# Performance work log

Measured on AMD Instinct MI355X. Metric: run time of the kernel, lower is better.

The kernel has to match this reference:

```python
import jax, jax.numpy as jnp
import numpy as np

B, L, E = 4, 2048, 1024
H, HS = 16, 64  # head_num, head_size; E == H*HS


def setup_inputs() -> dict:
    key = jax.random.key(0)
    k1, k2, k3 = jax.random.split(key, 3)
    x = jax.random.normal(k1, (B, L, E), dtype=jnp.float32)
    W_attn = jax.random.normal(k2, (E, 3 * H * HS), dtype=jnp.float32) * (E ** -0.5)
    W_ffn = jax.random.normal(k3, (H * HS, E), dtype=jnp.float32) * ((H * HS) ** -0.5)
    return {"x": x, "W_attn": W_attn, "W_ffn": W_ffn}


def reference(x, W_attn, W_ffn):
    b, l, _ = x.shape
    z = x @ W_attn  # [B, L, 3*H*HS]
    # NOTE: original splits as (k, q, v) in that order
    k, q, v = jnp.split(z, 3, axis=2)
    k = k.reshape(b, l, H, HS).transpose(0, 2, 1, 3)  # [B,H,L,HS]
    q = q.reshape(b, l, H, HS).transpose(0, 2, 1, 3)
    v = v.reshape(b, l, H, HS).transpose(0, 2, 1, 3)
    # scores[i, j] = k_i . q_j (k plays the row role, q the column role)
    scores = jnp.einsum('bhid,bhjd->bhij', k, q) / (HS ** 0.5)
    idx = jnp.arange(l)
    causal = idx[None, :] > idx[:, None]  # True where j > i (masked out)
    scores = jnp.where(causal[None, None], -jnp.inf, scores)
    attn = jax.nn.softmax(scores, axis=-1)  # softmax over j (the q index)
    y = jnp.einsum('bhij,bhjd->bhid', attn, v)  # [B,H,L,HS]
    y = y.transpose(0, 2, 1, 3).reshape(b, l, H * HS)
    return y @ W_ffn
```

## Files before the change

kernel.cpp:

```cpp
#include <hip/hip_runtime.h>
#include <hip/hip_bf16.h>

typedef __attribute__((ext_vector_type(8))) short bf16x8;
typedef __attribute__((ext_vector_type(4))) float f32x4;

__device__ __forceinline__ short f2b(float f) {
    unsigned u = __builtin_bit_cast(unsigned, f);
    unsigned r = (u + 0x7FFFu + ((u >> 16) & 1u)) >> 16;
    return (short)r;
}

__device__ __forceinline__ unsigned cvt_pk_bf16(float lo, float hi) {
    unsigned r;
    asm("v_cvt_pk_bf16_f32 %0, %1, %2" : "=v"(r) : "v"(lo), "v"(hi));
    return r;
}

__device__ __forceinline__ float fexp2(float x) {
    float r;
    asm("v_exp_f32 %0, %1" : "=v"(r) : "v"(x));
    return r;
}

__device__ __forceinline__ void gload_lds16(const void* g, void* l) {
    __builtin_amdgcn_global_load_lds((const __attribute__((address_space(1))) unsigned*)g,
                                     (__attribute__((address_space(3))) unsigned*)l, 16, 0, 0);
}

__global__ void conv_swz(const float* __restrict__ in, short* __restrict__ out, long nch) {
    long i = (long)blockIdx.x * blockDim.x + threadIdx.x;
    long stride = (long)gridDim.x * blockDim.x;
    for (; i < nch; i += stride) {
        long m = i >> 7;
        int ch = (int)(i & 127);
        int p = (ch & ~7) | ((ch ^ (int)m) & 7);
        const float4* s = (const float4*)(in + i * 8);
        float4 a = s[0], b = s[1];
        bf16x8 ov;
        ov[0] = f2b(a.x); ov[1] = f2b(a.y); ov[2] = f2b(a.z); ov[3] = f2b(a.w);
        ov[4] = f2b(b.x); ov[5] = f2b(b.y); ov[6] = f2b(b.z); ov[7] = f2b(b.w);
        *(bf16x8*)(out + (m << 10) + p * 8) = ov;
    }
}

__global__ void transpose_swz(const float* __restrict__ in, short* __restrict__ outT, int R, int C) {
    __shared__ float t[32][33];
    int c0 = blockIdx.x * 32, r0 = blockIdx.y * 32;
    int tx = threadIdx.x, ty = threadIdx.y;
    #pragma unroll
    for (int j = 0; j < 4; ++j)
        t[ty + j * 8][tx] = in[(long)(r0 + ty + j * 8) * C + c0 + tx];
    __syncthreads();
    #pragma unroll
    for (int j = 0; j < 4; ++j) {
        int n = c0 + ty + j * 8;
        int k = r0 + tx;
        int kp = (k & ~63) | ((((k >> 3) ^ n) & 7) << 3) | (k & 7);
        outT[(long)n * R + kp] = f2b(t[tx][ty + j * 8]);
    }
}

template<int MODE>
__launch_bounds__(256, 4)
__global__ void gemm_nt(const short* __restrict__ A, const short* __restrict__ Bt,
                        int M, int N, int K,
                        short* __restrict__ qrole, short* __restrict__ krole,
                        short* __restrict__ vT, float* __restrict__ out) {
    __shared__ __align__(16) short As[128][64];
    __shared__ __align__(16) short Bs[128][64];
    const int tid = threadIdx.x;
    const int lane = tid & 63;
    const int wid = tid >> 6;
    const int wm = wid >> 1, wn = wid & 1;
    const int m0 = blockIdx.y * 128, n0 = blockIdx.x * 128;
    const int r16 = lane & 15, g = lane >> 4;
    const int sw = r16 & 7;
    const char* Ab = (const char*)A;
    const char* Bb = (const char*)Bt;
    const long Kb = (long)K * 2;
    f32x4 acc[4][4] = {};
    for (int k0 = 0; k0 < K; k0 += 64) {
        #pragma unroll
        for (int it = 0; it < 4; ++it) {
            int id = it * 256 + tid;
            int r = id >> 3, cch = id & 7;
            gload_lds16(Ab + (long)(m0 + r) * Kb + k0 * 2 + cch * 16, (char*)As + id * 16);
            gload_lds16(Bb + (long)(n0 + r) * Kb + k0 * 2 + cch * 16, (char*)Bs + id * 16);
        }
        __syncthreads();
        #pragma unroll
        for (int kk = 0; kk < 2; ++kk) {
            bf16x8 af[4], bfr[4];
            #pragma unroll
            for (int m = 0; m < 4; ++m)
                af[m] = *(const bf16x8*)&As[wm * 64 + m * 16 + r16][((kk * 4 + g) ^ sw) * 8];
            #pragma unroll
            for (int n = 0; n < 4; ++n)
                bfr[n] = *(const bf16x8*)&Bs[wn * 64 + n * 16 + r16][((kk * 4 + g) ^ sw) * 8];
            #pragma unroll
            for (int m = 0; m < 4; ++m)
                #pragma unroll
                for (int n = 0; n < 4; ++n)
                    acc[m][n] = __builtin_amdgcn_mfma_f32_16x16x32_bf16(af[m], bfr[n], acc[m][n], 0, 0, 0);
        }
        __syncthreads();
    }
    #pragma unroll
    for (int m = 0; m < 4; ++m) {
        #pragma unroll
        for (int n = 0; n < 4; ++n) {
            #pragma unroll
            for (int r = 0; r < 4; ++r) {
                int row = m0 + wm * 64 + m * 16 + g * 4 + r;
                int col = n0 + wn * 64 + n * 16 + r16;
                float v = acc[m][n][r];
                if (MODE == 0) {
                    int which = col >> 10, cc = col & 1023;
                    int h = cc >> 6, d = cc & 63;
                    int b = row >> 11, li = row & 2047;
                    int bh = b * 16 + h;
                    if (which == 0)      qrole[((long)bh * 2048 + li) * 64 + d] = f2b(v * 0.18033688f);
                    else if (which == 1) krole[((long)bh * 2048 + li) * 64 + (d ^ ((li & 7) << 3))] = f2b(v);
                    else                 vT[((long)bh * 64 + d) * 2048 + ((li & ~63) | ((li & 63) ^ ((d & 7) << 3)))] = f2b(v);
                } else {
                    out[(long)row * N + col] = v;
                }
            }
        }
    }
}

__launch_bounds__(256, 4)
__global__ void attn_kernel(const short* __restrict__ qrole, const short* __restrict__ krole,
                            const short* __restrict__ vT, short* __restrict__ y) {
    __shared__ __align__(16) short K_lds[2][64][64];
    __shared__ __align__(16) short V_lds[2][64][64];
    __shared__ __align__(16) short P_lds[4][16][64];
    const int tid = threadIdx.x, lane = tid & 63, w = tid >> 6;
    const int r16 = lane & 15, g = lane >> 4;
    const int idb = blockIdx.x;
    const int bh = idb & 63;
    const int u = idb >> 8;
    const int a = (idb >> 6) & 3;
    const int c = (u == 0) ? (15 - a) : (u == 1) ? a : (u == 2) ? (11 - a) : (4 + a);
    const int q0 = c << 7;
    const int T = 2 * c + 2;
    const short* qb = qrole + (long)bh * (2048 * 64);
    const char* kbyte = (const char*)(krole + (long)bh * (2048 * 64));
    const char* vbyte = (const char*)(vT + (long)bh * (64 * 2048));
    const int b = bh >> 4, h = bh & 15;

    bf16x8 qf[2][2];
    #pragma unroll
    for (int m = 0; m < 2; ++m)
        #pragma unroll
        for (int ks = 0; ks < 2; ++ks)
            qf[m][ks] = *(const bf16x8*)&qb[(long)(q0 + m * 64 + w * 16 + r16) * 64 + ks * 32 + g * 8];

    f32x4 o[2][4] = {};
    float mr[2], lr[2];
    #pragma unroll
    for (int m = 0; m < 2; ++m) { mr[m] = -1e30f; lr[m] = 0.f; }

    const int rr = tid >> 3, cch = tid & 7;
    const char* kg0 = kbyte + rr * 128 + cch * 16;
    const char* kg1 = kbyte + (32 + rr) * 128 + cch * 16;
    const char* vg0 = vbyte + rr * 4096 + cch * 16;
    const char* vg1 = vbyte + (32 + rr) * 4096 + cch * 16;
    char* Kb_ = (char*)&K_lds[0][0][0];
    char* Vb_ = (char*)&V_lds[0][0][0];
    const int ld0 = tid * 16, ld1 = (256 + tid) * 16;

    gload_lds16(kg0, Kb_ + ld0);
    gload_lds16(kg1, Kb_ + ld1);
    gload_lds16(vg0, Vb_ + ld0);
    gload_lds16(vg1, Vb_ + ld1);

    const int psw = (r16 & 7) << 4;
    char* prow = (char*)&P_lds[w][r16][0];

    for (int t = 0; t < T; ++t) {
        __syncthreads();
        const int cur = t & 1;
        if (t + 1 < T) {
            long adv = (long)(t + 1) * 8192;
            long advv = (long)(t + 1) * 128;
            char* kdst = Kb_ + (cur ^ 1) * 8192;
            char* vdst = Vb_ + (cur ^ 1) * 8192;
            gload_lds16(kg0 + adv, kdst + ld0);
            gload_lds16(kg1 + adv, kdst + ld1);
            gload_lds16(vg0 + advv, vdst + ld0);
            gload_lds16(vg1 + advv, vdst + ld1);
        }
        const int jt = t << 6;
        const char* kbase = Kb_ + cur * 8192;
        const char* vbase = Vb_ + cur * 8192;

        #pragma unroll
        for (int m = 0; m < 2; ++m) {
            const int qbase = q0 + m * 64 + w * 16;
            if (jt > qbase + 15) continue;

            f32x4 s[4] = {};
            __builtin_amdgcn_s_setprio(1);
            #pragma unroll
            for (int ks = 0; ks < 2; ++ks)
                #pragma unroll
                for (int n = 0; n < 4; ++n) {
                    bf16x8 kf = *(const bf16x8*)(kbase + (n * 16 + r16) * 128 + ((ks * 64 + g * 16) ^ psw));
                    s[n] = __builtin_amdgcn_mfma_f32_16x16x32_bf16(kf, qf[m][ks], s[n], 0, 0, 0);
                }
            __builtin_amdgcn_s_setprio(0);
            if (jt + 63 > qbase) {
                const int i = qbase + r16;
                #pragma unroll
                for (int n = 0; n < 4; ++n)
                    #pragma unroll
                    for (int r = 0; r < 4; ++r)
                        if (jt + n * 16 + g * 4 + r > i) s[n][r] = -1e30f;
            }
            float t0 = fmaxf(fmaxf(s[0][0], s[0][1]), fmaxf(s[0][2], s[0][3]));
            float t1 = fmaxf(fmaxf(s[1][0], s[1][1]), fmaxf(s[1][2], s[1][3]));
            float t2 = fmaxf(fmaxf(s[2][0], s[2][1]), fmaxf(s[2][2], s[2][3]));
            float t3 = fmaxf(fmaxf(s[3][0], s[3][1]), fmaxf(s[3][2], s[3][3]));
            float tm = fmaxf(fmaxf(t0, t1), fmaxf(t2, t3));
            tm = fmaxf(tm, __shfl_xor(tm, 16));
            tm = fmaxf(tm, __shfl_xor(tm, 32));
            if (__any(tm > mr[m] + 11.5f)) {
                float mn = fmaxf(mr[m], tm);
                float sc = fexp2(mr[m] - mn);
                mr[m] = mn;
                lr[m] *= sc;
                float scr[4];
                #pragma unroll
                for (int r = 0; r < 4; ++r) scr[r] = __shfl(sc, (g << 2) + r);
                #pragma unroll
                for (int nd = 0; nd < 4; ++nd)
                    #pragma unroll
                    for (int r = 0; r < 4; ++r)
                        o[m][nd][r] *= scr[r];
            }
            float p[4][4];
            #pragma unroll
            for (int n = 0; n < 4; ++n) {
                p[n][0] = fexp2(s[n][0] - mr[m]);
                p[n][1] = fexp2(s[n][1] - mr[m]);
                p[n][2] = fexp2(s[n][2] - mr[m]);
                p[n][3] = fexp2(s[n][3] - mr[m]);
                unsigned w0 = cvt_pk_bf16(p[n][0], p[n][1]);
                unsigned w1 = cvt_pk_bf16(p[n][2], p[n][3]);
                unsigned long long dw = ((unsigned long long)w1 << 32) | w0;
                *(unsigned long long*)(prow + ((n * 32 + g * 8) ^ psw)) = dw;
            }
            float l0 = (p[0][0] + p[0][1]) + (p[0][2] + p[0][3]);
            float l1 = (p[1][0] + p[1][1]) + (p[1][2] + p[1][3]);
            float l2 = (p[2][0] + p[2][1]) + (p[2][2] + p[2][3]);
            float l3 = (p[3][0] + p[3][1]) + (p[3][2] + p[3][3]);
            float lsum = (l0 + l1) + (l2 + l3);
            lsum += __shfl_xor(lsum, 16);
            lsum += __shfl_xor(lsum, 32);
            lr[m] += lsum;
            __builtin_amdgcn_s_setprio(1);
            #pragma unroll
            for (int ks = 0; ks < 2; ++ks) {
                bf16x8 pf = *(const bf16x8*)(prow + ((ks * 64 + g * 16) ^ psw));
                #pragma unroll
                for (int nd = 0; nd < 4; ++nd) {
                    bf16x8 vf = *(const bf16x8*)(vbase + (nd * 16 + r16) * 128 + ((ks * 64 + g * 16) ^ psw));
                    o[m][nd] = __builtin_amdgcn_mfma_f32_16x16x32_bf16(pf, vf, o[m][nd], 0, 0, 0);
                }
            }
            __builtin_amdgcn_s_setprio(0);
        }
    }
    #pragma unroll
    for (int m = 0; m < 2; ++m) {
        float inv[4];
        #pragma unroll
        for (int r = 0; r < 4; ++r) inv[r] = 1.0f / __shfl(lr[m], (g << 2) + r);
        const int li0 = q0 + m * 64 + w * 16 + (g << 2);
        #pragma unroll
        for (int nd = 0; nd < 4; ++nd)
            #pragma unroll
            for (int r = 0; r < 4; ++r) {
                int li = li0 + r;
                int sub = ((nd * 2 + (r16 >> 3)) ^ li) & 7;
                int kp = h * 64 + sub * 8 + (r16 & 7);
                y[(long)(b * 2048 + li) * 1024 + kp] = f2b(o[m][nd][r] * inv[r]);
            }
    }
}

extern "C" void kernel_launch(void* const* d_in, const int* in_sizes, int n_in,
                              void* d_out, int out_size, void* d_ws, size_t ws_size,
                              hipStream_t stream) {
    const float* x  = (const float*)d_in[0];
    const float* Wa = (const float*)d_in[1];
    const float* Wf = (const float*)d_in[2];
    float* out = (float*)d_out;
    char* ws = (char*)d_ws;
    short* xb  = (short*)(ws);
    short* wab = (short*)(ws + (16l << 20));
    short* wfb = (short*)(ws + (22l << 20));
    short* qr  = (short*)(ws + (24l << 20));
    short* kr  = (short*)(ws + (40l << 20));
    short* vt  = (short*)(ws + (56l << 20));

    conv_swz<<<2048, 256, 0, stream>>>(x, xb, (long)8192 * 128);
    transpose_swz<<<dim3(96, 32), dim3(32, 8), 0, stream>>>(Wa, wab, 1024, 3072);
    transpose_swz<<<dim3(32, 32), dim3(32, 8), 0, stream>>>(Wf, wfb, 1024, 1024);
    gemm_nt<0><<<dim3(24, 64), 256, 0, stream>>>(xb, wab, 8192, 3072, 1024, qr, kr, vt, nullptr);
    attn_kernel<<<1024, 256, 0, stream>>>(qr, kr, vt, xb);
    gemm_nt<1><<<dim3(8, 64), 256, 0, stream>>>(xb, wfb, 8192, 1024, 1024, nullptr, nullptr, nullptr, out);
}
```

Measured before the change: 174.5 us.

## Split long causal query chunks across two blocks and merge partial softmax results

Query chunks 8-15 are each split into two KV-range segments handled by separate blocks, which write unnormalized bf16 partial outputs plus row max and sum to workspace. A new merge kernel rescales and combines each pair into y. This evens out per-block work under the causal mask and raises the block count to 1536, aiming to shorten the tail. The cost is an extra launch, extra global traffic, and bf16 rounding of the partial outputs. The split path only runs when the workspace is large enough.

```diff
diff --git a/kernel.cpp b/kernel.cpp
--- a/kernel.cpp
+++ b/kernel.cpp
@@ -8,6 +8,10 @@
     unsigned u = __builtin_bit_cast(unsigned, f);
     unsigned r = (u + 0x7FFFu + ((u >> 16) & 1u)) >> 16;
     return (short)r;
+}
+
+__device__ __forceinline__ float b2f(short s) {
+    return __builtin_bit_cast(float, ((unsigned)(unsigned short)s) << 16);
 }
 
 __device__ __forceinline__ unsigned cvt_pk_bf16(float lo, float hi) {
@@ -130,9 +134,14 @@
     }
 }
 
+__device__ const int g_uc[24]   = {15,15, 7,14,14, 6,13,13, 5,12,12, 4,11,11, 3,10,10, 2, 9, 9, 1, 8, 8, 0};
+__device__ const int g_ukind[24]= { 1, 2, 0, 1, 2, 0, 1, 2, 0, 1, 2, 0, 1, 2, 0, 1, 2, 0, 1, 2, 0, 1, 2, 0};
+
+template<int SPLIT>
 __launch_bounds__(256, 4)
 __global__ void attn_kernel(const short* __restrict__ qrole, const short* __restrict__ krole,
-                            const short* __restrict__ vT, short* __restrict__ y) {
+                            const short* __restrict__ vT, short* __restrict__ y,
+                            short* __restrict__ pO, float2* __restrict__ pML) {
     __shared__ __align__(16) short K_lds[2][64][64];
     __shared__ __align__(16) short V_lds[2][64][64];
     __shared__ __align__(16) short P_lds[4][16][64];
@@ -140,11 +149,19 @@
     const int r16 = lane & 15, g = lane >> 4;
     const int idb = blockIdx.x;
     const int bh = idb & 63;
-    const int u = idb >> 8;
-    const int a = (idb >> 6) & 3;
-    const int c = (u == 0) ? (15 - a) : (u == 1) ? a : (u == 2) ? (11 - a) : (4 + a);
+    int c, kind, t0, Tn;
+    if (SPLIT) {
+        const int u = idb >> 6;
+        c = g_uc[u];
+        kind = g_ukind[u];
+        t0 = (kind == 2) ? (c + 1) : 0;
+        Tn = (kind == 0) ? (2 * c + 2) : (c + 1);
+    } else {
+        const int u = idb >> 8, a = (idb >> 6) & 3;
+        c = (u == 0) ? (15 - a) : (u == 1) ? a : (u == 2) ? (11 - a) : (4 + a);
+        kind = 0; t0 = 0; Tn = 2 * c + 2;
+    }
     const int q0 = c << 7;
-    const int T = 2 * c + 2;
     const short* qb = qrole + (long)bh * (2048 * 64);
     const char* kbyte = (const char*)(krole + (long)bh * (2048 * 64));
     const char* vbyte = (const char*)(vT + (long)bh * (64 * 2048));
@@ -171,18 +188,19 @@
     char* Vb_ = (char*)&V_lds[0][0][0];
     const int ld0 = tid * 16, ld1 = (256 + tid) * 16;
 
-    gload_lds16(kg0, Kb_ + ld0);
-    gload_lds16(kg1, Kb_ + ld1);
-    gload_lds16(vg0, Vb_ + ld0);
-    gload_lds16(vg1, Vb_ + ld1);
+    gload_lds16(kg0 + (long)t0 * 8192, Kb_ + ld0);
+    gload_lds16(kg1 + (long)t0 * 8192, Kb_ + ld1);
+    gload_lds16(vg0 + (long)t0 * 128, Vb_ + ld0);
+    gload_lds16(vg1 + (long)t0 * 128, Vb_ + ld1);
 
     const int psw = (r16 & 7) << 4;
     char* prow = (char*)&P_lds[w][r16][0];
-
-    for (int t = 0; t < T; ++t) {
+    const int tend = t0 + Tn;
+
+    for (int t = t0; t < tend; ++t) {
         __syncthreads();
-        const int cur = t & 1;
-        if (t + 1 < T) {
+        const int cur = (t - t0) & 1;
+        if (t + 1 < tend) {
             long adv = (long)(t + 1) * 8192;
             long advv = (long)(t + 1) * 128;
             char* kdst = Kb_ + (cur ^ 1) * 8192;
@@ -211,7 +229,7 @@
                     s[n] = __builtin_amdgcn_mfma_f32_16x16x32_bf16(kf, qf[m][ks], s[n], 0, 0, 0);
                 }
             __builtin_amdgcn_s_setprio(0);
-            if (jt + 63 > qbase) {
+            if (kind != 1 && jt + 63 > qbase) {
                 const int i = qbase + r16;
                 #pragma unroll
                 for (int n = 0; n < 4; ++n)
@@ -219,11 +237,11 @@
                     for (int r = 0; r < 4; ++r)
                         if (jt + n * 16 + g * 4 + r > i) s[n][r] = -1e30f;
             }
-            float t0 = fmaxf(fmaxf(s[0][0], s[0][1]), fmaxf(s[0][2], s[0][3]));
-            float t1 = fmaxf(fmaxf(s[1][0], s[1][1]), fmaxf(s[1][2], s[1][3]));
-            float t2 = fmaxf(fmaxf(s[2][0], s[2][1]), fmaxf(s[2][2], s[2][3]));
-            float t3 = fmaxf(fmaxf(s[3][0], s[3][1]), fmaxf(s[3][2], s[3][3]));
-            float tm = fmaxf(fmaxf(t0, t1), fmaxf(t2, t3));
+            float t0_ = fmaxf(fmaxf(s[0][0], s[0][1]), fmaxf(s[0][2], s[0][3]));
+            float t1_ = fmaxf(fmaxf(s[1][0], s[1][1]), fmaxf(s[1][2], s[1][3]));
+            float t2_ = fmaxf(fmaxf(s[2][0], s[2][1]), fmaxf(s[2][2], s[2][3]));
+            float t3_ = fmaxf(fmaxf(s[3][0], s[3][1]), fmaxf(s[3][2], s[3][3]));
+            float tm = fmaxf(fmaxf(t0_, t1_), fmaxf(t2_, t3_));
             tm = fmaxf(tm, __shfl_xor(tm, 16));
             tm = fmaxf(tm, __shfl_xor(tm, 32));
             if (__any(tm > mr[m] + 11.5f)) {
@@ -273,21 +291,75 @@
             __builtin_amdgcn_s_setprio(0);
         }
     }
-    #pragma unroll
-    for (int m = 0; m < 2; ++m) {
-        float inv[4];
-        #pragma unroll
-        for (int r = 0; r < 4; ++r) inv[r] = 1.0f / __shfl(lr[m], (g << 2) + r);
-        const int li0 = q0 + m * 64 + w * 16 + (g << 2);
-        #pragma unroll
-        for (int nd = 0; nd < 4; ++nd)
+
+    if (kind == 0) {
+        #pragma unroll
+        for (int m = 0; m < 2; ++m) {
+            float inv[4];
+            #pragma unroll
+            for (int r = 0; r < 4; ++r) inv[r] = 1.0f / __shfl(lr[m], (g << 2) + r);
+            const int li0 = q0 + m * 64 + w * 16 + (g << 2);
+            #pragma unroll
+            for (int nd = 0; nd < 4; ++nd)
+                #pragma unroll
+                for (int r = 0; r < 4; ++r) {
+                    int li = li0 + r;
+                    int sub = ((nd * 2 + (r16 >> 3)) ^ li) & 7;
+                    int kp = h * 64 + sub * 8 + (r16 & 7);
+                    y[(long)(b * 2048 + li) * 1024 + kp] = f2b(o[m][nd][r] * inv[r]);
+                }
+        }
+    } else {
+        const int seg = kind - 1, sc_ = c - 8;
+        const long slot = ((long)bh * 8 + sc_) * 2 + seg;
+        #pragma unroll
+        for (int m = 0; m < 2; ++m) {
+            float mv[4], lv[4];
             #pragma unroll
             for (int r = 0; r < 4; ++r) {
-                int li = li0 + r;
-                int sub = ((nd * 2 + (r16 >> 3)) ^ li) & 7;
-                int kp = h * 64 + sub * 8 + (r16 & 7);
-                y[(long)(b * 2048 + li) * 1024 + kp] = f2b(o[m][nd][r] * inv[r]);
-            }
+                mv[r] = __shfl(mr[m], (g << 2) + r);
+                lv[r] = __shfl(lr[m], (g << 2) + r);
+            }
+            const int row0 = m * 64 + w * 16 + (g << 2);
+            #pragma unroll
+            for (int nd = 0; nd < 4; ++nd)
+                #pragma unroll
+                for (int r = 0; r < 4; ++r)
+                    pO[(slot * 128 + row0 + r) * 64 + nd * 16 + r16] = f2b(o[m][nd][r]);
+            if (r16 == 0) {
+                #pragma unroll
+                for (int r = 0; r < 4; ++r)
+                    pML[slot * 128 + row0 + r] = make_float2(mv[r], lv[r]);
+            }
+        }
+    }
+}
+
+__global__ void merge_kernel(const short* __restrict__ pO, const float2* __restrict__ pML,
+                             short* __restrict__ y) {
+    const int bh = blockIdx.x >> 3, sc_ = blockIdx.x & 7;
+    const int row = threadIdx.x >> 1, hf = threadIdx.x & 1;
+    const long slotA = ((long)bh * 8 + sc_) * 2, slotB = slotA + 1;
+    const float2 mlA = pML[slotA * 128 + row];
+    const float2 mlB = pML[slotB * 128 + row];
+    const float ms = fmaxf(mlA.x, mlB.x);
+    const float eA = fexp2(mlA.x - ms), eB = fexp2(mlB.x - ms);
+    const float inv = 1.0f / (mlA.y * eA + mlB.y * eB);
+    const float fA = eA * inv, fB = eB * inv;
+    const int c = 8 + sc_;
+    const int li = (c << 7) + row;
+    const int b = bh >> 4, h = bh & 15;
+    #pragma unroll
+    for (int ch = 0; ch < 4; ++ch) {
+        const int d0 = hf * 32 + ch * 8;
+        bf16x8 a = *(const bf16x8*)&pO[(slotA * 128 + row) * 64 + d0];
+        bf16x8 bb = *(const bf16x8*)&pO[(slotB * 128 + row) * 64 + d0];
+        bf16x8 res;
+        #pragma unroll
+        for (int j = 0; j < 8; ++j)
+            res[j] = f2b(b2f(a[j]) * fA + b2f(bb[j]) * fB);
+        const int kp0 = h * 64 + ((((d0 >> 3) ^ li) & 7) << 3);
+        *(bf16x8*)&y[(long)(b * 2048 + li) * 1024 + kp0] = res;
     }
 }
 
@@ -305,11 +377,18 @@
     short* qr  = (short*)(ws + (24l << 20));
     short* kr  = (short*)(ws + (40l << 20));
     short* vt  = (short*)(ws + (56l << 20));
+    short* pO  = (short*)(ws + (72l << 20));
+    float2* pML = (float2*)(ws + (89l << 20));
 
     conv_swz<<<2048, 256, 0, stream>>>(x, xb, (long)8192 * 128);
     transpose_swz<<<dim3(96, 32), dim3(32, 8), 0, stream>>>(Wa, wab, 1024, 3072);
     transpose_swz<<<dim3(32, 32), dim3(32, 8), 0, stream>>>(Wf, wfb, 1024, 1024);
     gemm_nt<0><<<dim3(24, 64), 256, 0, stream>>>(xb, wab, 8192, 3072, 1024, qr, kr, vt, nullptr);
-    attn_kernel<<<1024, 256, 0, stream>>>(qr, kr, vt, xb);
+    if (ws_size >= (91ull << 20)) {
+        attn_kernel<1><<<1536, 256, 0, stream>>>(qr, kr, vt, xb, pO, pML);
+        merge_kernel<<<512, 256, 0, stream>>>(pO, pML, xb);
+    } else {
+        attn_kernel<0><<<1024, 256, 0, stream>>>(qr, kr, vt, xb, nullptr, nullptr);
+    }
     gemm_nt<1><<<dim3(8, 64), 256, 0, stream>>>(xb, wfb, 8192, 1024, 1024, nullptr, nullptr, nullptr, out);
 }
```

Result: slower. 182.0 us (+4.3%).

## Use 256x256-tile double-buffered GEMM kernel for QKV projection

Applied to the files above, without the earlier changes.

Replaces the 128x128 QKV projection GEMM with a dedicated 512-thread kernel using 256x256 output tiles, 128KB of double-buffered LDS filled by direct global-to-LDS loads, and an interleaved stage/read/MFMA schedule with priority hints. Blocks are remapped across M/N for better cache locality. The larger tile cuts global and LDS traffic per FLOP and overlaps loads with compute, at the cost of one block per CU and only 384 blocks for 256 CUs, which leaves a wave-quantization tail. The output GEMM is de-templated, and some attention variables are renamed.

```diff
diff --git a/kernel.cpp b/kernel.cpp
--- a/kernel.cpp
+++ b/kernel.cpp
@@ -60,12 +60,130 @@
     }
 }
 
-template<int MODE>
+__launch_bounds__(512, 1)
+__global__ void gemm256_nt(const short* __restrict__ A, const short* __restrict__ Bt,
+                           short* __restrict__ qrole, short* __restrict__ krole,
+                           short* __restrict__ vT) {
+    __shared__ __align__(16) char ldsb[131072];
+    const int tid = threadIdx.x, lane = tid & 63, wid = tid >> 6;
+    const int wm = wid >> 2, wn = wid & 3;
+    const int r16 = lane & 15, g = lane >> 4;
+    const int sw8 = r16 & 7;
+    const int swz = (blockIdx.x & 7) * 48 + (blockIdx.x >> 3);
+    const int m0 = (swz & 31) * 256, n0 = (swz >> 5) * 256;
+    const long Kb2 = 2048;
+    const char* Ab = (const char*)A;
+    const char* Bb = (const char*)Bt;
+    const int c0 = tid, c1 = tid + 512;
+    const int sr0 = c0 >> 3, so0 = (c0 & 7) * 16;
+    const int sr1 = c1 >> 3, so1 = (c1 & 7) * 16;
+
+    f32x4 acc[8][4] = {};
+    bf16x8 af[4][2], bfr[4][2];
+
+#define STAGE_A(tt, h) do { \
+        const char* sb_ = Ab + (long)(m0 + (h) * 128) * Kb2 + (long)(tt) * 128; \
+        char* db_ = ldsb + ((tt) & 1) * 65536 + (h) * 16384; \
+        gload_lds16(sb_ + (long)sr0 * Kb2 + so0, db_ + c0 * 16); \
+        gload_lds16(sb_ + (long)sr1 * Kb2 + so1, db_ + c1 * 16); } while (0)
+#define STAGE_B(tt, h) do { \
+        const char* sb_ = Bb + (long)(n0 + (h) * 128) * Kb2 + (long)(tt) * 128; \
+        char* db_ = ldsb + ((tt) & 1) * 65536 + 32768 + (h) * 16384; \
+        gload_lds16(sb_ + (long)sr0 * Kb2 + so0, db_ + c0 * 16); \
+        gload_lds16(sb_ + (long)sr1 * Kb2 + so1, db_ + c1 * 16); } while (0)
+#define READ_A(buf, mh) do { \
+        const char* base_ = ldsb + (buf) * 65536; \
+        _Pragma("unroll") \
+        for (int f_ = 0; f_ < 4; ++f_) { \
+            const char* rp_ = base_ + (wm * 128 + (mh) * 64 + f_ * 16 + r16) * 128; \
+            af[f_][0] = *(const bf16x8*)(rp_ + ((g ^ sw8) * 16)); \
+            af[f_][1] = *(const bf16x8*)(rp_ + (((4 + g) ^ sw8) * 16)); } } while (0)
+#define READ_B(buf) do { \
+        const char* base_ = ldsb + (buf) * 65536 + 32768; \
+        _Pragma("unroll") \
+        for (int f_ = 0; f_ < 4; ++f_) { \
+            const char* rp_ = base_ + (wn * 64 + f_ * 16 + r16) * 128; \
+            bfr[f_][0] = *(const bf16x8*)(rp_ + ((g ^ sw8) * 16)); \
+            bfr[f_][1] = *(const bf16x8*)(rp_ + (((4 + g) ^ sw8) * 16)); } } while (0)
+#define DO_MFMA(mh, nh) do { \
+        __builtin_amdgcn_s_setprio(1); \
+        _Pragma("unroll") \
+        for (int f_ = 0; f_ < 4; ++f_) \
+            _Pragma("unroll") \
+            for (int n_ = 0; n_ < 2; ++n_) { \
+                acc[(mh) * 4 + f_][(nh) * 2 + n_] = __builtin_amdgcn_mfma_f32_16x16x32_bf16( \
+                    af[f_][0], bfr[(nh) * 2 + n_][0], acc[(mh) * 4 + f_][(nh) * 2 + n_], 0, 0, 0); \
+                acc[(mh) * 4 + f_][(nh) * 2 + n_] = __builtin_amdgcn_mfma_f32_16x16x32_bf16( \
+                    af[f_][1], bfr[(nh) * 2 + n_][1], acc[(mh) * 4 + f_][(nh) * 2 + n_], 0, 0, 0); } \
+        __builtin_amdgcn_s_setprio(0); } while (0)
+#define BAR() __builtin_amdgcn_s_barrier()
+
+    STAGE_B(0, 0); STAGE_B(0, 1); STAGE_A(0, 0); STAGE_A(0, 1);
+    STAGE_B(1, 0); STAGE_B(1, 1); STAGE_A(1, 0);
+    asm volatile("s_waitcnt vmcnt(6)" ::: "memory");
+    BAR();
+
+    for (int i = 0; i < 8; ++i) {
+        const int t = 2 * i;
+        const bool nl = (i < 7);
+        READ_A(0, 0); READ_B(0);
+        STAGE_A(t + 1, 1);
+        BAR(); DO_MFMA(0, 0); BAR();
+        if (nl) STAGE_B(t + 2, 0);
+        BAR(); DO_MFMA(0, 1); BAR();
+        READ_A(0, 1);
+        if (nl) STAGE_B(t + 2, 1);
+        BAR(); DO_MFMA(1, 0); BAR();
+        if (nl) STAGE_A(t + 2, 0);
+        BAR(); DO_MFMA(1, 1);
+        if (nl) asm volatile("s_waitcnt vmcnt(6)" ::: "memory");
+        else    asm volatile("s_waitcnt vmcnt(0)" ::: "memory");
+        BAR();
+        READ_A(1, 0); READ_B(1);
+        if (nl) STAGE_A(t + 2, 1);
+        BAR(); DO_MFMA(0, 0); BAR();
+        if (nl) STAGE_B(t + 3, 0);
+        BAR(); DO_MFMA(0, 1); BAR();
+        READ_A(1, 1);
+        if (nl) STAGE_B(t + 3, 1);
+        BAR(); DO_MFMA(1, 0); BAR();
+        if (nl) STAGE_A(t + 3, 0);
+        BAR(); DO_MFMA(1, 1);
+        if (nl) asm volatile("s_waitcnt vmcnt(6)" ::: "memory");
+        else    asm volatile("s_waitcnt vmcnt(0)" ::: "memory");
+        BAR();
+    }
+#undef STAGE_A
+#undef STAGE_B
+#undef READ_A
+#undef READ_B
+#undef DO_MFMA
+#undef BAR
+
+    #pragma unroll
+    for (int m = 0; m < 8; ++m) {
+        #pragma unroll
+        for (int n = 0; n < 4; ++n) {
+            #pragma unroll
+            for (int r = 0; r < 4; ++r) {
+                int row = m0 + wm * 128 + m * 16 + g * 4 + r;
+                int col = n0 + wn * 64 + n * 16 + r16;
+                float v = acc[m][n][r];
+                int which = col >> 10, cc = col & 1023;
+                int h = cc >> 6, d = cc & 63;
+                int b = row >> 11, li = row & 2047;
+                int bh = b * 16 + h;
+                if (which == 0)      qrole[((long)bh * 2048 + li) * 64 + d] = f2b(v * 0.18033688f);
+                else if (which == 1) krole[((long)bh * 2048 + li) * 64 + (d ^ ((li & 7) << 3))] = f2b(v);
+                else                 vT[((long)bh * 64 + d) * 2048 + ((li & ~63) | ((li & 63) ^ ((d & 7) << 3)))] = f2b(v);
+            }
+        }
+    }
+}
+
 __launch_bounds__(256, 4)
 __global__ void gemm_nt(const short* __restrict__ A, const short* __restrict__ Bt,
-                        int M, int N, int K,
-                        short* __restrict__ qrole, short* __restrict__ krole,
-                        short* __restrict__ vT, float* __restrict__ out) {
+                        int M, int N, int K, float* __restrict__ out) {
     __shared__ __align__(16) short As[128][64];
     __shared__ __align__(16) short Bs[128][64];
     const int tid = threadIdx.x;
@@ -106,28 +224,15 @@
         __syncthreads();
     }
     #pragma unroll
-    for (int m = 0; m < 4; ++m) {
-        #pragma unroll
-        for (int n = 0; n < 4; ++n) {
+    for (int m = 0; m < 4; ++m)
+        #pragma unroll
+        for (int n = 0; n < 4; ++n)
             #pragma unroll
             for (int r = 0; r < 4; ++r) {
                 int row = m0 + wm * 64 + m * 16 + g * 4 + r;
                 int col = n0 + wn * 64 + n * 16 + r16;
-                float v = acc[m][n][r];
-                if (MODE == 0) {
-                    int which = col >> 10, cc = col & 1023;
-                    int h = cc >> 6, d = cc & 63;
-                    int b = row >> 11, li = row & 2047;
-                    int bh = b * 16 + h;
-                    if (which == 0)      qrole[((long)bh * 2048 + li) * 64 + d] = f2b(v * 0.18033688f);
-                    else if (which == 1) krole[((long)bh * 2048 + li) * 64 + (d ^ ((li & 7) << 3))] = f2b(v);
-                    else                 vT[((long)bh * 64 + d) * 2048 + ((li & ~63) | ((li & 63) ^ ((d & 7) << 3)))] = f2b(v);
-                } else {
-                    out[(long)row * N + col] = v;
-                }
-            }
-        }
-    }
+                out[(long)row * N + col] = acc[m][n][r];
+            }
 }
 
 __launch_bounds__(256, 4)
@@ -219,11 +324,11 @@
                     for (int r = 0; r < 4; ++r)
                         if (jt + n * 16 + g * 4 + r > i) s[n][r] = -1e30f;
             }
-            float t0 = fmaxf(fmaxf(s[0][0], s[0][1]), fmaxf(s[0][2], s[0][3]));
-            float t1 = fmaxf(fmaxf(s[1][0], s[1][1]), fmaxf(s[1][2], s[1][3]));
-            float t2 = fmaxf(fmaxf(s[2][0], s[2][1]), fmaxf(s[2][2], s[2][3]));
-            float t3 = fmaxf(fmaxf(s[3][0], s[3][1]), fmaxf(s[3][2], s[3][3]));
-            float tm = fmaxf(fmaxf(t0, t1), fmaxf(t2, t3));
+            float t0_ = fmaxf(fmaxf(s[0][0], s[0][1]), fmaxf(s[0][2], s[0][3]));
+            float t1_ = fmaxf(fmaxf(s[1][0], s[1][1]), fmaxf(s[1][2], s[1][3]));
+            float t2_ = fmaxf(fmaxf(s[2][0], s[2][1]), fmaxf(s[2][2], s[2][3]));
+            float t3_ = fmaxf(fmaxf(s[3][0], s[3][1]), fmaxf(s[3][2], s[3][3]));
+            float tm = fmaxf(fmaxf(t0_, t1_), fmaxf(t2_, t3_));
             tm = fmaxf(tm, __shfl_xor(tm, 16));
             tm = fmaxf(tm, __shfl_xor(tm, 32));
             if (__any(tm > mr[m] + 11.5f)) {
@@ -309,7 +414,7 @@
     conv_swz<<<2048, 256, 0, stream>>>(x, xb, (long)8192 * 128);
     transpose_swz<<<dim3(96, 32), dim3(32, 8), 0, stream>>>(Wa, wab, 1024, 3072);
     transpose_swz<<<dim3(32, 32), dim3(32, 8), 0, stream>>>(Wf, wfb, 1024, 1024);
-    gemm_nt<0><<<dim3(24, 64), 256, 0, stream>>>(xb, wab, 8192, 3072, 1024, qr, kr, vt, nullptr);
+    gemm256_nt<<<384, 512, 0, stream>>>(xb, wab, qr, kr, vt);
     attn_kernel<<<1024, 256, 0, stream>>>(qr, kr, vt, xb);
-    gemm_nt<1><<<dim3(8, 64), 256, 0, stream>>>(xb, wfb, 8192, 1024, 1024, nullptr, nullptr, nullptr, out);
-}
+    gemm_nt<<<dim3(8, 64), 256, 0, stream>>>(xb, wfb, 8192, 1024, 1024, out);
+}
```

Measured after the change: 199.5 us. +14.3%, slower.
